# Optimization experiments

Hardware: AMD Instinct MI355X
Metric: run time of the kernel (lower is better)

## Reference

```python
import jax, jax.numpy as jnp
import numpy as np

B, C_IN, T = 16, 1, 10240
C = 256                # conv_dim_out == config.model.conv_channels
KERNEL, STRIDE, PAD = 10, 5, 0
K_STEPS = 12           # config.model.predict_steps
NEG = 10               # config.train.neg_samples
EPS = 1e-5
L_OUT = (T + 2 * PAD - KERNEL) // STRIDE + 1   # 2047


def setup_inputs() -> dict:
    key = jax.random.key(0)
    ks = jax.random.split(key, 5)
    return {
        "x": jax.random.normal(ks[0], (B, C_IN, T), jnp.float32),
        "conv_w": jax.random.normal(ks[1], (C, C_IN, KERNEL), jnp.float32) * 0.1,
        "conv_b": jnp.zeros((C,), jnp.float32),
        "bn_gamma": jnp.ones((C,), jnp.float32),
        "bn_beta": jnp.zeros((C,), jnp.float32),
        "tr_w": jax.random.normal(ks[2], (K_STEPS, C, C), jnp.float32) / np.sqrt(C).astype(np.float32),
        "tr_b": jnp.zeros((K_STEPS, C), jnp.float32),
        "perm": jax.random.permutation(ks[3], L_OUT),  # randperm over the time axis
    }


def reference(x, conv_w, conv_b, bn_gamma, bn_beta, tr_w, tr_b, perm):
    # ---- encoder: Conv1d -> ReLU -> BatchNorm1d (training-mode batch stats) ----
    h = jax.lax.conv_general_dilated(
        x, conv_w, window_strides=(STRIDE,), padding=[(PAD, PAD)],
        dimension_numbers=("NCH", "OIH", "NCH"))
    h = jax.nn.relu(h + conv_b[None, :, None])            # (B, C, L)
    mu = h.mean(axis=(0, 2), keepdims=True)
    var = h.var(axis=(0, 2), keepdims=True)               # biased, as torch BN
    h = (h - mu) * jax.lax.rsqrt(var + EPS)
    h = h * bn_gamma[None, :, None] + bn_beta[None, :, None]
    z = h.transpose(0, 2, 1)                              # (B, L, C)

    # ---- negatives: batch-roll by 1, random permutation of the time axis; detached ----
    z_negative = jax.lax.stop_gradient(jnp.roll(z, 1, axis=0)[:, perm, :])

    L = z.shape[1]
    # z_neg_full[b, i] == roll(z_neg, i, axis=0)[b] == z_neg[(b - i) % B]
    roll_idx = (jnp.arange(B)[:, None] - jnp.arange(NEG)[None, :]) % B  # (B, NEG)

    losses = []
    for k in range(1, K_STEPS + 1):
        l_len = L - k
        z_pos = z[:, k:, :]                               # (B, l, C)
        z_neg = z_negative[:, k:, :]                      # (B, l, C)
        z_neg_full = z_neg[roll_idx]                      # (B, NEG, l, C)
        W, bb = tr_w[k - 1], tr_b[k - 1]
        est_pos = (z_pos @ W + bb)[:, None]               # (B, 1, l, C)
        est_neg = z_neg_full @ W + bb                     # (B, NEG, l, C)
        estimated = jnp.concatenate([est_pos, est_neg], axis=1)        # (B, S, l, C)
        z_full = jnp.concatenate([z_pos[:, None], z_neg_full], axis=1)  # (B, S, l, C)
        f = jnp.einsum("bslc,bslc->bsl", estimated, z_full)
        # faithful to torch: flatten (b, s, l) row-major then view as (b*l, S)
        f_k = f.reshape(B * l_len, NEG + 1)
        logp = jax.nn.log_softmax(f_k, axis=1)
        losses.append(-logp.sum() / ((l_len - k) * B))

    # torch forward returns z.permute(0, 2, 1); losses returned too for baseline use
    return z.transpose(0, 2, 1), jnp.stack(losses)
```

## Files before the change

### kernel.cpp

```cpp
#include <hip/hip_runtime.h>
#include <hip/hip_bf16.h>
#include <math.h>

constexpr int B_ = 16;
constexpr int T_ = 10240;
constexpr int C_ = 256;
constexpr int KW = 10;
constexpr int L_ = 2047;
constexpr int N_ = B_ * L_;
constexpr int KSTEPS = 12;
constexpr float EPS_ = 1e-5f;
constexpr int QSTR = 32768;

typedef short bf16x8 __attribute__((ext_vector_type(8)));
typedef float f32x4  __attribute__((ext_vector_type(4)));

__global__ __launch_bounds__(256) void stats_wt_kernel(
    const float* __restrict__ x, const float* __restrict__ cw, const float* __restrict__ cb,
    float* __restrict__ ssum, float* __restrict__ ssq,
    const float* __restrict__ tw, __hip_bfloat16* __restrict__ Wt)
{
    __shared__ float smem[64 * 65];
    const int bid = blockIdx.x;
    if (bid < 256) {
        const int b  = bid & 15;
        const int l0 = (bid >> 4) * 128;
        const int cnt = min(128, L_ - l0);
        const int c = threadIdx.x;
        float* xs = smem;
        const float* xb = x + (size_t)b * T_;
        for (int i = threadIdx.x; i < cnt * 5 + 5; i += 256) xs[i] = xb[l0 * 5 + i];
        float w[KW];
#pragma unroll
        for (int j = 0; j < KW; ++j) w[j] = cw[c * KW + j];
        const float bias = cb[c];
        __syncthreads();
        float s = 0.f, s2 = 0.f;
        for (int dl = 0; dl < cnt; ++dl) {
            float v = bias;
#pragma unroll
            for (int j = 0; j < KW; ++j) v = fmaf(xs[dl * 5 + j], w[j], v);
            v = fmaxf(v, 0.f);
            s += v;
            s2 = fmaf(v, v, s2);
        }
        atomicAdd(&ssum[c], s);
        atomicAdd(&ssq[c], s2);
    } else {
        const int idx = bid - 256;
        const int k  = idx >> 4;
        const int c0 = ((idx & 15) >> 2) * 64, j0 = (idx & 3) * 64;
        float (*tile)[65] = (float(*)[65])smem;
        for (int i = threadIdx.x; i < 64 * 64; i += 256) {
            int c = i >> 6, j = i & 63;
            tile[c][j] = tw[((size_t)k * C_ + (c0 + c)) * C_ + j0 + j];
        }
        __syncthreads();
        for (int i = threadIdx.x; i < 64 * 64; i += 256) {
            int j = i >> 6, c = i & 63;
            Wt[((size_t)k * C_ + (j0 + j)) * C_ + c0 + c] = __float2bfloat16(tile[c][j]);
        }
    }
}

__global__ __launch_bounds__(256) void conv_norm_kernel(
    const float* __restrict__ x, const float* __restrict__ cw, const float* __restrict__ cb,
    const float* __restrict__ ssum, const float* __restrict__ ssq,
    const float* __restrict__ gamma, const float* __restrict__ beta,
    __hip_bfloat16* __restrict__ Zb, float* __restrict__ out0)
{
    const int b  = blockIdx.y;
    const int l0 = blockIdx.x * 32;
    const int cnt = min(32, L_ - l0);
    const int c = threadIdx.x;
    __shared__ float xs[32 * 5 + 8];
    __shared__ float zt[32][257];
    const float* xb = x + (size_t)b * T_;
    for (int i = threadIdx.x; i < cnt * 5 + 5; i += 256) xs[i] = xb[l0 * 5 + i];
    float w[KW];
#pragma unroll
    for (int j = 0; j < KW; ++j) w[j] = cw[c * KW + j];
    const float bias = cb[c];
    const float inv_n = 1.0f / (float)N_;
    const float mu  = ssum[c] * inv_n;
    const float var = ssq[c] * inv_n - mu * mu;
    const float sc  = gamma[c] * rsqrtf(var + EPS_);
    const float sh  = beta[c] - mu * sc;
    __syncthreads();
    for (int dl = 0; dl < cnt; ++dl) {
        float v = bias;
#pragma unroll
        for (int j = 0; j < KW; ++j) v = fmaf(xs[dl * 5 + j], w[j], v);
        v = fmaxf(v, 0.f);
        float z = fmaf(v, sc, sh);
        Zb[((size_t)(b * L_ + l0 + dl)) * C_ + c] = __float2bfloat16(z);
        zt[dl][c] = z;
    }
    __syncthreads();
    const int lq  = threadIdx.x & 31;
    const int cr0 = threadIdx.x >> 5;
    if (lq < cnt) {
#pragma unroll
        for (int i = 0; i < 32; ++i) {
            int cr = cr0 * 32 + i;
            out0[((size_t)(b * C_ + cr)) * L_ + l0 + lq] = zt[lq][cr];
        }
    }
}

__global__ __launch_bounds__(512, 4) void qmfma_kernel(
    const __hip_bfloat16* __restrict__ Zb, const __hip_bfloat16* __restrict__ Wt,
    const float* __restrict__ tb, float* __restrict__ qt)
{
    const int k   = blockIdx.y;
    const int grp = blockIdx.x;
    const __hip_bfloat16* __restrict__ Wk = Wt + (size_t)k * C_ * C_;

    __shared__ __hip_bfloat16 zs[4][32 * 256];
    __shared__ float qacc[8][256];

    const int tid  = threadIdx.x;
    const int lane = tid & 63, wave = tid >> 6;
    const int n16  = lane & 15, quad = lane >> 4;
    const int sw   = n16 & 7;
    const int row0 = grp * 8 * 32;

    bf16x8 wfrag[2][8];
    {
        const __hip_bfloat16* wb = Wk + ((size_t)(32 * wave + n16)) * C_ + quad * 8;
#pragma unroll
        for (int ct = 0; ct < 2; ++ct)
#pragma unroll
            for (int it = 0; it < 8; ++it)
                wfrag[ct][it] = *(const bf16x8*)(wb + ct * 16 * C_ + it * 32);
    }
    float4 bias4[2];
#pragma unroll
    for (int ct = 0; ct < 2; ++ct)
        bias4[ct] = *(const float4*)(tb + k * C_ + 32 * wave + ct * 16 + quad * 4);

#define STAGE(buf, t) do {                                                                  \
    _Pragma("unroll")                                                                       \
    for (int i_ = 0; i_ < 2; ++i_) {                                                        \
        int ch = i_ * 512 + wave * 64 + lane;                                               \
        int rr = ch >> 5;                                                                   \
        int rg = row0 + (t) * 32 + rr; if (rg > N_ - 1) rg = N_ - 1;                        \
        int jj = (lane & 31) ^ (rr & 7);                                                    \
        __builtin_amdgcn_global_load_lds(                                                   \
            (const __attribute__((address_space(1))) void*)(Zb + (size_t)rg * C_ + jj * 8), \
            (__attribute__((address_space(3))) void*)(&zs[buf][i_ * 4096 + wave * 512]),    \
            16, 0, 0);                                                                      \
    }                                                                                       \
} while (0)

    STAGE(0, 0);
    STAGE(1, 1);
    asm volatile("s_waitcnt vmcnt(0)" ::: "memory");

#pragma unroll
    for (int t = 0; t < 8; ++t) {
        if (t < 6) STAGE((t + 2) & 3, t + 2);
        if (t < 6)                { asm volatile("s_waitcnt vmcnt(4)" ::: "memory"); }
        else if (t == 6)          { asm volatile("s_waitcnt vmcnt(2)" ::: "memory"); }
        else                      { asm volatile("s_waitcnt vmcnt(0)" ::: "memory"); }
        __builtin_amdgcn_s_barrier();

        const __hip_bfloat16* zsp = (const __hip_bfloat16*)zs[t & 3];

        f32x4 acc[2][2];
#pragma unroll
        for (int rt = 0; rt < 2; ++rt)
#pragma unroll
            for (int ct = 0; ct < 2; ++ct) acc[rt][ct] = f32x4{0.f, 0.f, 0.f, 0.f};

        __builtin_amdgcn_s_setprio(1);
#pragma unroll
        for (int it = 0; it < 8; ++it) {
            const int js = (it * 4 + quad) ^ sw;
            bf16x8 zf0 = *(const bf16x8*)(zsp + n16 * 256 + js * 8);
            bf16x8 zf1 = *(const bf16x8*)(zsp + (n16 + 16) * 256 + js * 8);
#pragma unroll
            for (int ct = 0; ct < 2; ++ct) {
                acc[0][ct] = __builtin_amdgcn_mfma_f32_16x16x32_bf16(
                    wfrag[ct][it], zf0, acc[0][ct], 0, 0, 0);
                acc[1][ct] = __builtin_amdgcn_mfma_f32_16x16x32_bf16(
                    wfrag[ct][it], zf1, acc[1][ct], 0, 0, 0);
            }
        }
        __builtin_amdgcn_s_setprio(0);

#pragma unroll
        for (int rt = 0; rt < 2; ++rt) {
            const int row = rt * 16 + n16;
            float s = 0.f;
#pragma unroll
            for (int ct = 0; ct < 2; ++ct) {
                const int j  = 4 * wave + 2 * ct + (quad >> 1);
                const char* zp = (const char*)zsp + row * 512 + ((j ^ sw) << 4) + (quad & 1) * 8;
                uint2 zz = *(const uint2*)zp;
                float z0 = __uint_as_float(zz.x << 16);
                float z1 = __uint_as_float(zz.x & 0xffff0000u);
                float z2 = __uint_as_float(zz.y << 16);
                float z3 = __uint_as_float(zz.y & 0xffff0000u);
                s = fmaf(acc[rt][ct][0] + bias4[ct].x, z0, s);
                s = fmaf(acc[rt][ct][1] + bias4[ct].y, z1, s);
                s = fmaf(acc[rt][ct][2] + bias4[ct].z, z2, s);
                s = fmaf(acc[rt][ct][3] + bias4[ct].w, z3, s);
            }
            s += __shfl_xor(s, 16);
            s += __shfl_xor(s, 32);
            if (lane < 16) qacc[wave][t * 32 + row] = s;
        }
    }
#undef STAGE

    __syncthreads();
    if (tid < 256) {
        int rg = row0 + tid;
        if (rg < N_) {
            float qv = 0.f;
#pragma unroll
            for (int w2 = 0; w2 < 8; ++w2) qv += qacc[w2][tid];
            int b = rg / L_;
            int l = rg - b * L_;
            qt[(size_t)k * QSTR + (l << 4) + b] = qv;
        }
    }
}

__global__ __launch_bounds__(256) void loss_kernel(
    const float* __restrict__ qt, const int* __restrict__ perm, float* __restrict__ lacc)
{
    const int k = blockIdx.y + 1;
    const float* qk = qt + (size_t)(k - 1) * QSTR;
    const int nval = B_ * (L_ - k);
    const int idx = blockIdx.x * 256 + threadIdx.x;

    float contrib = 0.f;
    if (idx < nval) {
        int b = idx & 15;
        int l = k + (idx >> 4);
        float f0 = qk[(l << 4) | b];
        int pl = perm[l];
        const float* qn = qk + ((size_t)pl << 4);
        float f[10];
#pragma unroll
        for (int n = 0; n < 10; ++n) f[n] = qn[(b + 15 - n) & 15];
        float m = f0;
#pragma unroll
        for (int i = 0; i < 10; ++i) m = fmaxf(m, f[i]);
        float se = __expf(f0 - m), fs = f0;
#pragma unroll
        for (int i = 0; i < 10; ++i) { se += __expf(f[i] - m); fs += f[i]; }
        contrib = 11.f * (m + __logf(se)) - fs;
    }

    __shared__ float red[4];
#pragma unroll
    for (int off = 32; off > 0; off >>= 1) contrib += __shfl_down(contrib, off);
    const int lane = threadIdx.x & 63;
    const int wave = threadIdx.x >> 6;
    if (lane == 0) red[wave] = contrib;
    __syncthreads();
    if (threadIdx.x == 0) atomicAdd(&lacc[k - 1], red[0] + red[1] + red[2] + red[3]);
}

__global__ void finalize_loss_kernel(const float* __restrict__ lacc, float* __restrict__ out1)
{
    int k = threadIdx.x;
    if (k < KSTEPS) {
        float div = (float)((L_ - 2 * (k + 1)) * B_);
        out1[k] = lacc[k] / div;
    }
}

extern "C" void kernel_launch(void* const* d_in, const int* in_sizes, int n_in,
                              void* d_out, int out_size, void* d_ws, size_t ws_size,
                              hipStream_t stream)
{
    const float* x     = (const float*)d_in[0];
    const float* cw    = (const float*)d_in[1];
    const float* cb    = (const float*)d_in[2];
    const float* gamma = (const float*)d_in[3];
    const float* beta  = (const float*)d_in[4];
    const float* tw    = (const float*)d_in[5];
    const float* tb    = (const float*)d_in[6];
    const int*   perm  = (const int*)d_in[7];

    float* out0 = (float*)d_out;
    float* out1 = out0 + (size_t)B_ * C_ * L_;

    char* ws = (char*)d_ws;
    __hip_bfloat16* Zb = (__hip_bfloat16*)ws;   ws += (size_t)N_ * C_ * 2;
    __hip_bfloat16* Wt = (__hip_bfloat16*)ws;   ws += (size_t)KSTEPS * C_ * C_ * 2;
    float* qt    = (float*)ws;                  ws += (size_t)KSTEPS * QSTR * 4;
    float* ssum  = (float*)ws;                  ws += C_ * 4;
    float* ssq   = (float*)ws;                  ws += C_ * 4;
    float* lacc  = (float*)ws;                  ws += 64 * 4;

    hipMemsetAsync(ssum, 0, (C_ + C_ + 64) * sizeof(float), stream);

    stats_wt_kernel<<<448, 256, 0, stream>>>(x, cw, cb, ssum, ssq, tw, Wt);

    dim3 gcv(64, 16);
    conv_norm_kernel<<<gcv, 256, 0, stream>>>(x, cw, cb, ssum, ssq, gamma, beta, Zb, out0);

    dim3 gq(128, KSTEPS);
    qmfma_kernel<<<gq, 512, 0, stream>>>(Zb, Wt, tb, qt);

    dim3 gl(128, KSTEPS);
    loss_kernel<<<gl, 256, 0, stream>>>(qt, perm, lacc);
    finalize_loss_kernel<<<1, 64, 0, stream>>>(lacc, out1);
}
```

Measured before the change: 188.6 us.

## Replace atomic stat/loss accumulation with per-block reductions and drop memset

The BN stats part of stats_wt_kernel now gives each block one channel, loops over all batches with the full input row staged in shared memory, and writes the channel sum directly instead of using atomics. The loss kernel writes per-block partials that a 768-thread finalize kernel reduces per step. Together these remove the hipMemsetAsync and every float atomic, which also makes the results deterministic. In exchange, each stats block recomputes the conv for every batch and position of its channel and uses 40KB of shared memory, which may limit occupancy.

```diff
diff --git a/kernel.cpp b/kernel.cpp
--- a/kernel.cpp
+++ b/kernel.cpp
@@ -20,43 +20,58 @@
     float* __restrict__ ssum, float* __restrict__ ssq,
     const float* __restrict__ tw, __hip_bfloat16* __restrict__ Wt)
 {
-    __shared__ float smem[64 * 65];
+    __shared__ float smem[T_];
+    __shared__ float redS[4], redQ[4];
     const int bid = blockIdx.x;
+    const int tid = threadIdx.x;
     if (bid < 256) {
-        const int b  = bid & 15;
-        const int l0 = (bid >> 4) * 128;
-        const int cnt = min(128, L_ - l0);
-        const int c = threadIdx.x;
-        float* xs = smem;
-        const float* xb = x + (size_t)b * T_;
-        for (int i = threadIdx.x; i < cnt * 5 + 5; i += 256) xs[i] = xb[l0 * 5 + i];
+        const int c = bid;
         float w[KW];
 #pragma unroll
         for (int j = 0; j < KW; ++j) w[j] = cw[c * KW + j];
         const float bias = cb[c];
+        float s = 0.f, s2 = 0.f;
+        for (int b = 0; b < B_; ++b) {
+            __syncthreads();
+            const float4* xb4 = (const float4*)(x + (size_t)b * T_);
+            for (int i = tid; i < T_ / 4; i += 256) ((float4*)smem)[i] = xb4[i];
+            __syncthreads();
+#pragma unroll
+            for (int i = 0; i < 8; ++i) {
+                int l = i * 256 + tid;
+                if (l < L_) {
+                    float v = bias;
+#pragma unroll
+                    for (int j = 0; j < KW; ++j) v = fmaf(smem[l * 5 + j], w[j], v);
+                    v = fmaxf(v, 0.f);
+                    s += v;
+                    s2 = fmaf(v, v, s2);
+                }
+            }
+        }
+#pragma unroll
+        for (int off = 32; off > 0; off >>= 1) {
+            s  += __shfl_down(s, off);
+            s2 += __shfl_down(s2, off);
+        }
+        const int lane = tid & 63, wave = tid >> 6;
+        if (lane == 0) { redS[wave] = s; redQ[wave] = s2; }
         __syncthreads();
-        float s = 0.f, s2 = 0.f;
-        for (int dl = 0; dl < cnt; ++dl) {
-            float v = bias;
-#pragma unroll
-            for (int j = 0; j < KW; ++j) v = fmaf(xs[dl * 5 + j], w[j], v);
-            v = fmaxf(v, 0.f);
-            s += v;
-            s2 = fmaf(v, v, s2);
-        }
-        atomicAdd(&ssum[c], s);
-        atomicAdd(&ssq[c], s2);
+        if (tid == 0) {
+            ssum[c] = redS[0] + redS[1] + redS[2] + redS[3];
+            ssq[c]  = redQ[0] + redQ[1] + redQ[2] + redQ[3];
+        }
     } else {
         const int idx = bid - 256;
         const int k  = idx >> 4;
         const int c0 = ((idx & 15) >> 2) * 64, j0 = (idx & 3) * 64;
         float (*tile)[65] = (float(*)[65])smem;
-        for (int i = threadIdx.x; i < 64 * 64; i += 256) {
+        for (int i = tid; i < 64 * 64; i += 256) {
             int c = i >> 6, j = i & 63;
             tile[c][j] = tw[((size_t)k * C_ + (c0 + c)) * C_ + j0 + j];
         }
         __syncthreads();
-        for (int i = threadIdx.x; i < 64 * 64; i += 256) {
+        for (int i = tid; i < 64 * 64; i += 256) {
             int j = i >> 6, c = i & 63;
             Wt[((size_t)k * C_ + (j0 + j)) * C_ + c0 + c] = __float2bfloat16(tile[c][j]);
         }
@@ -229,7 +244,7 @@
 }
 
 __global__ __launch_bounds__(256) void loss_kernel(
-    const float* __restrict__ qt, const int* __restrict__ perm, float* __restrict__ lacc)
+    const float* __restrict__ qt, const int* __restrict__ perm, float* __restrict__ lpart)
 {
     const int k = blockIdx.y + 1;
     const float* qk = qt + (size_t)(k - 1) * QSTR;
@@ -262,15 +277,21 @@
     const int wave = threadIdx.x >> 6;
     if (lane == 0) red[wave] = contrib;
     __syncthreads();
-    if (threadIdx.x == 0) atomicAdd(&lacc[k - 1], red[0] + red[1] + red[2] + red[3]);
-}
-
-__global__ void finalize_loss_kernel(const float* __restrict__ lacc, float* __restrict__ out1)
-{
-    int k = threadIdx.x;
-    if (k < KSTEPS) {
-        float div = (float)((L_ - 2 * (k + 1)) * B_);
-        out1[k] = lacc[k] / div;
+    if (threadIdx.x == 0)
+        lpart[(size_t)(k - 1) * 128 + blockIdx.x] = red[0] + red[1] + red[2] + red[3];
+}
+
+__global__ __launch_bounds__(768) void finalize_loss_kernel(
+    const float* __restrict__ lpart, float* __restrict__ out1)
+{
+    const int w = threadIdx.x >> 6;
+    const int lane = threadIdx.x & 63;
+    float v = lpart[(size_t)w * 128 + lane] + lpart[(size_t)w * 128 + lane + 64];
+#pragma unroll
+    for (int off = 32; off > 0; off >>= 1) v += __shfl_down(v, off);
+    if (lane == 0) {
+        float div = (float)((L_ - 2 * (w + 1)) * B_);
+        out1[w] = v / div;
     }
 }
 
@@ -296,9 +317,7 @@
     float* qt    = (float*)ws;                  ws += (size_t)KSTEPS * QSTR * 4;
     float* ssum  = (float*)ws;                  ws += C_ * 4;
     float* ssq   = (float*)ws;                  ws += C_ * 4;
-    float* lacc  = (float*)ws;                  ws += 64 * 4;
-
-    hipMemsetAsync(ssum, 0, (C_ + C_ + 64) * sizeof(float), stream);
+    float* lpart = (float*)ws;                  ws += (size_t)KSTEPS * 128 * 4;
 
     stats_wt_kernel<<<448, 256, 0, stream>>>(x, cw, cb, ssum, ssq, tw, Wt);
 
@@ -309,6 +328,6 @@
     qmfma_kernel<<<gq, 512, 0, stream>>>(Zb, Wt, tb, qt);
 
     dim3 gl(128, KSTEPS);
-    loss_kernel<<<gl, 256, 0, stream>>>(qt, perm, lacc);
-    finalize_loss_kernel<<<1, 64, 0, stream>>>(lacc, out1);
-}
+    loss_kernel<<<gl, 256, 0, stream>>>(qt, perm, lpart);
+    finalize_loss_kernel<<<1, 768, 0, stream>>>(lpart, out1);
+}
```

After: 208.6 us. 1.11x slower.
